# Kernel tuning notes

Hardware: AMD Instinct MI355X
Metric: run time of the kernel (lower is better)

Reference implementation:

```python
import jax, jax.numpy as jnp
import numpy as np

G, N, E, F_IN, F_OUT, C = 256, 512, 4096, 64, 64, 16


def setup_inputs() -> dict:
    key = jax.random.key(0)
    ks = jax.random.split(key, 6)
    x_batch = jax.random.normal(ks[0], (G, N, F_IN), dtype=jnp.float32)
    edge_index_batch = jax.random.randint(ks[1], (G, 2, E), 0, N, dtype=jnp.int32)
    conv_weight = jax.random.normal(ks[2], (F_OUT, F_IN), dtype=jnp.float32) * (1.0 / np.sqrt(F_IN))
    conv_bias = jax.random.normal(ks[3], (F_OUT,), dtype=jnp.float32) * 0.02
    lin_weight = jax.random.normal(ks[4], (C, F_OUT * N), dtype=jnp.float32) * (1.0 / np.sqrt(F_OUT * N))
    lin_bias = jax.random.normal(ks[5], (C,), dtype=jnp.float32) * 0.02
    return {"x_batch": x_batch, "edge_index_batch": edge_index_batch,
            "conv_weight": conv_weight, "conv_bias": conv_bias,
            "lin_weight": lin_weight, "lin_bias": lin_bias}


def _gcn_conv_graph(xw, edge_index, self_loops):
    # xw: [N, F_OUT] (already linearly transformed), edge_index: [2, E]
    row = jnp.concatenate([edge_index[0], self_loops])  # sources
    col = jnp.concatenate([edge_index[1], self_loops])  # targets
    ones = jnp.ones(row.shape[0], dtype=xw.dtype)
    deg = jax.ops.segment_sum(ones, col, num_segments=N)  # degree at target nodes
    dinv = jnp.where(deg > 0, jax.lax.rsqrt(deg), jnp.zeros_like(deg))
    norm = dinv[row] * dinv[col]                          # [E+N]
    msgs = xw[row] * norm[:, None]                        # gather + normalize
    return jax.ops.segment_sum(msgs, col, num_segments=N)  # scatter-add at targets


def reference(x_batch, edge_index_batch, conv_weight, conv_bias, lin_weight, lin_bias):
    # GCNConv (PyG defaults: self-loops, symmetric normalization, post-agg bias)
    xw = jnp.einsum('gnf,of->gno', x_batch, conv_weight)  # [G, N, F_OUT]
    self_loops = jnp.arange(N, dtype=edge_index_batch.dtype)
    h = jax.vmap(_gcn_conv_graph, in_axes=(0, 0, None))(xw, edge_index_batch, self_loops)
    h = h + conv_bias
    h = jax.nn.relu(h)
    flat = h.reshape(h.shape[0], -1)                      # [G, N*F_OUT]
    logits = flat @ lin_weight.T + lin_bias               # [G, C]
    return jax.nn.log_softmax(logits, axis=-1)
```

## Files before the change

kernel.cpp:

```cpp
#include <hip/hip_runtime.h>

#define Gn 256
#define Nn 512
#define En 4096
#define Fn 64
#define Cn 16
#define ET (En + Nn)

typedef _Float16 halfv8 __attribute__((ext_vector_type(8)));
typedef _Float16 halfv4 __attribute__((ext_vector_type(4)));
typedef _Float16 halfv2 __attribute__((ext_vector_type(2)));
typedef float    f32x4  __attribute__((ext_vector_type(4)));

__device__ __forceinline__ float pk_norm(unsigned p) {
    return (float)__builtin_bit_cast(_Float16, (unsigned short)(p & 0xffffu));
}

__global__ __launch_bounds__(256) void cvt_lw(
    const float* __restrict__ lw,
    _Float16* __restrict__ lwh)
{
    const int i = blockIdx.x * 256 + threadIdx.x;
    float4 a = *((const float4*)lw + (size_t)i * 2);
    float4 b = *((const float4*)lw + (size_t)i * 2 + 1);
    halfv8 hv;
    hv[0]=(_Float16)a.x; hv[1]=(_Float16)a.y; hv[2]=(_Float16)a.z; hv[3]=(_Float16)a.w;
    hv[4]=(_Float16)b.x; hv[5]=(_Float16)b.y; hv[6]=(_Float16)b.z; hv[7]=(_Float16)b.w;
    *(halfv8*)(lwh + (size_t)i * 8) = hv;
}

__global__ __launch_bounds__(1024, 4) void gcn_fused(
    const float* __restrict__ x,
    const int*   __restrict__ ei,
    const float* __restrict__ w,
    const float* __restrict__ wbias,
    const _Float16* __restrict__ lwh,
    const float* __restrict__ lbias,
    float* __restrict__ out)
{
    __shared__ unsigned short xs_h[Nn * Fn];
    __shared__ unsigned short xhs[Nn * Fn];
    __shared__ unsigned short wts[Fn * Fn];
    __shared__ unsigned int   epk[ET + 8];
    __shared__ float dinv[Nn];
    __shared__ int   cnt[Nn];
    __shared__ int   wsum[8];

    const int g    = blockIdx.x;
    const int tid  = threadIdx.x;
    const int lane = tid & 63;
    const int wid  = tid >> 6;

    const float* xg = x + (size_t)g * Nn * Fn;
    const int*   es = ei + (size_t)g * 2 * En;
    const int*   ed = es + En;

    const int e0s = es[tid], e1s = es[tid + 1024], e2s = es[tid + 2048], e3s = es[tid + 3072];
    const int e0t = ed[tid], e1t = ed[tid + 1024], e2t = ed[tid + 2048], e3t = ed[tid + 3072];

    if (tid < Nn) dinv[tid] = 1.0f;
    __syncthreads();

    atomicAdd(&dinv[e0t], 1.0f);
    atomicAdd(&dinv[e1t], 1.0f);
    atomicAdd(&dinv[e2t], 1.0f);
    atomicAdd(&dinv[e3t], 1.0f);

    float4 xv[8];
    #pragma unroll
    for (int it = 0; it < 8; ++it) xv[it] = *(const float4*)(xg + (tid + it * 1024) * 4);
    __syncthreads();

    int c = 0;
    if (tid < Nn) { float d = dinv[tid]; c = (int)d; dinv[tid] = rsqrtf(d); }
    int v_ = c;
    #pragma unroll
    for (int off = 1; off < 64; off <<= 1) {
        int u = __shfl_up(v_, off, 64);
        if (lane >= off) v_ += u;
    }
    if (wid < 8 && lane == 63) wsum[wid] = v_;
    __syncthreads();
    if (tid == 0) { int a = 0; for (int i = 0; i < 8; ++i) { int t = wsum[i]; wsum[i] = a; a += t; } }
    __syncthreads();
    if (tid < Nn) cnt[tid] = v_ - c + wsum[wid];
    __syncthreads();

    {
        #define FILL_EDGE(ss, tt) { \
            float nrm = dinv[ss] * dinv[tt]; \
            int slot = atomicAdd(&cnt[tt], 1); \
            unsigned short nb = __builtin_bit_cast(unsigned short, (_Float16)nrm); \
            epk[slot] = ((unsigned)(ss) << 16) | nb; }
        FILL_EDGE(e0s, e0t)
        FILL_EDGE(e1s, e1t)
        FILL_EDGE(e2s, e2t)
        FILL_EDGE(e3s, e3t)
        #undef FILL_EDGE
        if (tid < Nn) {
            float dv = dinv[tid];
            float nrm = dv * dv;
            int slot = atomicAdd(&cnt[tid], 1);
            unsigned short nb = __builtin_bit_cast(unsigned short, (_Float16)nrm);
            epk[slot] = ((unsigned)tid << 16) | nb;
        }
    }

    {
        int o = tid >> 4, f0 = (tid & 15) * 4;
        float4 v = *(const float4*)(w + o * Fn + f0);
        halfv4 hv; hv[0]=(_Float16)v.x; hv[1]=(_Float16)v.y;
                   hv[2]=(_Float16)v.z; hv[3]=(_Float16)v.w;
        int blk = f0 >> 3, hf = (f0 >> 2) & 1;
        *(halfv4*)((char*)wts + o * 128 + ((blk ^ (o & 7)) * 16) + hf * 8) = hv;
    }

    #pragma unroll
    for (int it = 0; it < 8; ++it) {
        int idx = tid + it * 1024;
        float4 v = xv[it];
        halfv4 hv; hv[0]=(_Float16)v.x; hv[1]=(_Float16)v.y;
                   hv[2]=(_Float16)v.z; hv[3]=(_Float16)v.w;
        *(halfv4*)((char*)xs_h + idx * 8) = hv;
    }
    __syncthreads();

    {
        const int qid = lane >> 4, fl = lane & 15;
        for (int r = 0; r < 8; ++r) {
            int t = r * 64 + wid * 4 + qid;
            int beg = (t == 0) ? 0 : cnt[t - 1];
            int end = cnt[t];
            float a0 = 0.f, a1 = 0.f, a2 = 0.f, a3 = 0.f;
            unsigned pA0 = epk[beg],     pA1 = epk[beg + 1];
            unsigned pA2 = epk[beg + 2], pA3 = epk[beg + 3];
            int j = beg;
            for (; j + 4 <= end; j += 4) {
                unsigned pB0 = epk[j + 4], pB1 = epk[j + 5];
                unsigned pB2 = epk[j + 6], pB3 = epk[j + 7];
                int s0 = pA0 >> 16, s1 = pA1 >> 16, s2 = pA2 >> 16, s3 = pA3 >> 16;
                float n0 = pk_norm(pA0), n1 = pk_norm(pA1);
                float n2 = pk_norm(pA2), n3 = pk_norm(pA3);
                halfv4 x0 = *(const halfv4*)((const char*)xs_h + s0 * 128 + fl * 8);
                halfv4 x1 = *(const halfv4*)((const char*)xs_h + s1 * 128 + fl * 8);
                halfv4 x2 = *(const halfv4*)((const char*)xs_h + s2 * 128 + fl * 8);
                halfv4 x3 = *(const halfv4*)((const char*)xs_h + s3 * 128 + fl * 8);
                a0 += n0 * (float)x0[0] + n1 * (float)x1[0] + n2 * (float)x2[0] + n3 * (float)x3[0];
                a1 += n0 * (float)x0[1] + n1 * (float)x1[1] + n2 * (float)x2[1] + n3 * (float)x3[1];
                a2 += n0 * (float)x0[2] + n1 * (float)x1[2] + n2 * (float)x2[2] + n3 * (float)x3[2];
                a3 += n0 * (float)x0[3] + n1 * (float)x1[3] + n2 * (float)x2[3] + n3 * (float)x3[3];
                pA0 = pB0; pA1 = pB1; pA2 = pB2; pA3 = pB3;
            }
            for (; j < end; ++j) {
                int s = pA0 >> 16;
                float nm = pk_norm(pA0);
                halfv4 xvv = *(const halfv4*)((const char*)xs_h + s * 128 + fl * 8);
                a0 += nm * (float)xvv[0]; a1 += nm * (float)xvv[1];
                a2 += nm * (float)xvv[2]; a3 += nm * (float)xvv[3];
                pA0 = pA1; pA1 = pA2; pA2 = pA3;
            }
            halfv4 hv; hv[0]=(_Float16)a0; hv[1]=(_Float16)a1;
                       hv[2]=(_Float16)a2; hv[3]=(_Float16)a3;
            int dw = t * 32 + (((fl >> 1) ^ (t & 7)) * 4) + (fl & 1) * 2;
            *(halfv4*)((char*)xhs + dw * 4) = hv;
        }
    }
    __syncthreads();

    {
        const int m = lane & 15, q = lane >> 4;
        #pragma unroll
        for (int j = 0; j < 8; ++j) {
            int idx = wid * 8 + j, tm = idx >> 2, to = idx & 3;
            int n = tm * 16 + m, o = to * 16 + m;
            halfv8 X0 = *(const halfv8*)((const char*)xhs + n * 128 + ((q       ^ (n & 7)) * 16));
            halfv8 X1 = *(const halfv8*)((const char*)xhs + n * 128 + (((4 + q) ^ (n & 7)) * 16));
            halfv8 W0 = *(const halfv8*)((const char*)wts + o * 128 + ((q       ^ (o & 7)) * 16));
            halfv8 W1 = *(const halfv8*)((const char*)wts + o * 128 + (((4 + q) ^ (o & 7)) * 16));
            f32x4 acc = {0.f, 0.f, 0.f, 0.f};
            acc = __builtin_amdgcn_mfma_f32_16x16x32_f16(W0, X0, acc, 0, 0, 0);
            acc = __builtin_amdgcn_mfma_f32_16x16x32_f16(W1, X1, acc, 0, 0, 0);
            float4 bq = *(const float4*)&wbias[to * 16 + q * 4];
            halfv4 hv;
            hv[0] = (_Float16)fmaxf(acc[0] + bq.x, 0.0f);
            hv[1] = (_Float16)fmaxf(acc[1] + bq.y, 0.0f);
            hv[2] = (_Float16)fmaxf(acc[2] + bq.z, 0.0f);
            hv[3] = (_Float16)fmaxf(acc[3] + bq.w, 0.0f);
            int sw = (to * 4 + q) ^ m;
            *(halfv4*)((char*)xs_h + n * 128 + sw * 8) = hv;
        }
    }
    __syncthreads();

    {
        const _Float16* lwc = lwh + (size_t)wid * (Nn * Fn);
        const int l7 = lane & 7, l3 = lane >> 3;
        float acc = 0.f;
        #pragma unroll 4
        for (int i = 0; i < 64; ++i) {
            int n  = i * 8 + l3;
            int rb = n << 7;
            int sA = ((l7 * 2)     ^ (n & 15));
            int sB = ((l7 * 2 + 1) ^ (n & 15));
            halfv4 hA = *(const halfv4*)((const char*)xs_h + rb + sA * 8);
            halfv4 hB = *(const halfv4*)((const char*)xs_h + rb + sB * 8);
            halfv8 wv8 = *(const halfv8*)(lwc + (n << 6) + l7 * 8);
#if __has_builtin(__builtin_amdgcn_fdot2)
            halfv2 a0; a0[0]=hA[0]; a0[1]=hA[1];
            halfv2 a1; a1[0]=hA[2]; a1[1]=hA[3];
            halfv2 a2; a2[0]=hB[0]; a2[1]=hB[1];
            halfv2 a3; a3[0]=hB[2]; a3[1]=hB[3];
            halfv2 b0; b0[0]=wv8[0]; b0[1]=wv8[1];
            halfv2 b1; b1[0]=wv8[2]; b1[1]=wv8[3];
            halfv2 b2; b2[0]=wv8[4]; b2[1]=wv8[5];
            halfv2 b3; b3[0]=wv8[6]; b3[1]=wv8[7];
            acc = __builtin_amdgcn_fdot2(a0, b0, acc, false);
            acc = __builtin_amdgcn_fdot2(a1, b1, acc, false);
            acc = __builtin_amdgcn_fdot2(a2, b2, acc, false);
            acc = __builtin_amdgcn_fdot2(a3, b3, acc, false);
#else
            acc += (float)hA[0]*(float)wv8[0] + (float)hA[1]*(float)wv8[1]
                 + (float)hA[2]*(float)wv8[2] + (float)hA[3]*(float)wv8[3]
                 + (float)hB[0]*(float)wv8[4] + (float)hB[1]*(float)wv8[5]
                 + (float)hB[2]*(float)wv8[6] + (float)hB[3]*(float)wv8[7];
#endif
        }
        #pragma unroll
        for (int off = 32; off > 0; off >>= 1) acc += __shfl_xor(acc, off, 64);
        if (lane == 0) dinv[wid] = acc;
    }
    __syncthreads();

    if (tid < Cn) {
        float v = dinv[tid] + lbias[tid];
        float m = v;
        #pragma unroll
        for (int off = 8; off > 0; off >>= 1) m = fmaxf(m, __shfl_xor(m, off, 16));
        float ex = expf(v - m);
        float ssum = ex;
        #pragma unroll
        for (int off = 8; off > 0; off >>= 1) ssum += __shfl_xor(ssum, off, 16);
        out[g * Cn + tid] = v - m - logf(ssum);
    }
}

extern "C" void kernel_launch(void* const* d_in, const int* in_sizes, int n_in,
                              void* d_out, int out_size, void* d_ws, size_t ws_size,
                              hipStream_t stream) {
    const float* x  = (const float*)d_in[0];
    const int*   ei = (const int*)d_in[1];
    const float* w  = (const float*)d_in[2];
    const float* wb = (const float*)d_in[3];
    const float* lw = (const float*)d_in[4];
    const float* lb = (const float*)d_in[5];
    float* out = (float*)d_out;

    _Float16* lwh = (_Float16*)d_ws;

    hipLaunchKernelGGL(cvt_lw, dim3(256), dim3(256), 0, stream, lw, lwh);
    hipLaunchKernelGGL(gcn_fused, dim3(Gn), dim3(1024), 0, stream,
                       x, ei, w, wb, lwh, lb, out);
}
```

Before: 112.6 us.

## Hoist global loads early, prefetch linear weights, use LDS-only barriers

Moves the x, conv weight and linear bias global loads to the start of the kernel so they overlap with the degree-count atomics. It also prefetches the first eight linear-weight vectors before the MFMA stage and keeps an eight-deep register ring buffer of them in the final dot-product loop. __syncthreads is replaced with a barrier that waits only on LDS counters, so in-flight global loads are not drained at each barrier. The final stage reads one 16-byte LDS vector per row instead of two 8-byte ones, which requires remapping weight element order. The cost is higher register pressure at 1024 threads per block, and the partial-wait barrier is correct only while no barrier-ordered dependency goes through global memory.

```diff
diff --git a/kernel.cpp b/kernel.cpp
--- a/kernel.cpp
+++ b/kernel.cpp
@@ -14,6 +14,12 @@
 
 __device__ __forceinline__ float pk_norm(unsigned p) {
     return (float)__builtin_bit_cast(_Float16, (unsigned short)(p & 0xffffu));
+}
+
+__device__ __forceinline__ void bar_lds() {
+    asm volatile("s_waitcnt lgkmcnt(0)" ::: "memory");
+    __builtin_amdgcn_s_barrier();
+    __builtin_amdgcn_sched_barrier(0);
 }
 
 __global__ __launch_bounds__(256) void cvt_lw(
@@ -57,19 +63,20 @@
 
     const int e0s = es[tid], e1s = es[tid + 1024], e2s = es[tid + 2048], e3s = es[tid + 3072];
     const int e0t = ed[tid], e1t = ed[tid + 1024], e2t = ed[tid + 2048], e3t = ed[tid + 3072];
+    float4 xv[8];
+    #pragma unroll
+    for (int it = 0; it < 8; ++it) xv[it] = *(const float4*)(xg + (tid + it * 1024) * 4);
+    const float4 wv = *(const float4*)(w + (tid >> 4) * Fn + (tid & 15) * 4);
+    const float lbv = (tid < Cn) ? lbias[tid] : 0.0f;
 
     if (tid < Nn) dinv[tid] = 1.0f;
-    __syncthreads();
+    bar_lds();
 
     atomicAdd(&dinv[e0t], 1.0f);
     atomicAdd(&dinv[e1t], 1.0f);
     atomicAdd(&dinv[e2t], 1.0f);
     atomicAdd(&dinv[e3t], 1.0f);
-
-    float4 xv[8];
-    #pragma unroll
-    for (int it = 0; it < 8; ++it) xv[it] = *(const float4*)(xg + (tid + it * 1024) * 4);
-    __syncthreads();
+    bar_lds();
 
     int c = 0;
     if (tid < Nn) { float d = dinv[tid]; c = (int)d; dinv[tid] = rsqrtf(d); }
@@ -80,11 +87,11 @@
         if (lane >= off) v_ += u;
     }
     if (wid < 8 && lane == 63) wsum[wid] = v_;
-    __syncthreads();
+    bar_lds();
     if (tid == 0) { int a = 0; for (int i = 0; i < 8; ++i) { int t = wsum[i]; wsum[i] = a; a += t; } }
-    __syncthreads();
+    bar_lds();
     if (tid < Nn) cnt[tid] = v_ - c + wsum[wid];
-    __syncthreads();
+    bar_lds();
 
     {
         #define FILL_EDGE(ss, tt) { \
@@ -108,9 +115,8 @@
 
     {
         int o = tid >> 4, f0 = (tid & 15) * 4;
-        float4 v = *(const float4*)(w + o * Fn + f0);
-        halfv4 hv; hv[0]=(_Float16)v.x; hv[1]=(_Float16)v.y;
-                   hv[2]=(_Float16)v.z; hv[3]=(_Float16)v.w;
+        halfv4 hv; hv[0]=(_Float16)wv.x; hv[1]=(_Float16)wv.y;
+                   hv[2]=(_Float16)wv.z; hv[3]=(_Float16)wv.w;
         int blk = f0 >> 3, hf = (f0 >> 2) & 1;
         *(halfv4*)((char*)wts + o * 128 + ((blk ^ (o & 7)) * 16) + hf * 8) = hv;
     }
@@ -123,7 +129,7 @@
                    hv[2]=(_Float16)v.z; hv[3]=(_Float16)v.w;
         *(halfv4*)((char*)xs_h + idx * 8) = hv;
     }
-    __syncthreads();
+    bar_lds();
 
     {
         const int qid = lane >> 4, fl = lane & 15;
@@ -165,7 +171,15 @@
             *(halfv4*)((char*)xhs + dw * 4) = hv;
         }
     }
-    __syncthreads();
+
+    const _Float16* lwc = lwh + (size_t)wid * (Nn * Fn);
+    const int l7 = lane & 7, l3 = lane >> 3;
+    const _Float16* lwp_base = lwc + l3 * 64 + l7 * 8;
+    halfv8 lwp[8];
+    #pragma unroll
+    for (int p = 0; p < 8; ++p) lwp[p] = *(const halfv8*)(lwp_base + p * 512);
+
+    bar_lds();
 
     {
         const int m = lane & 15, q = lane >> 4;
@@ -190,49 +204,46 @@
             *(halfv4*)((char*)xs_h + n * 128 + sw * 8) = hv;
         }
     }
-    __syncthreads();
-
-    {
-        const _Float16* lwc = lwh + (size_t)wid * (Nn * Fn);
-        const int l7 = lane & 7, l3 = lane >> 3;
+    bar_lds();
+
+    {
+        const int woA = (l3 & 1) * 4;
         float acc = 0.f;
-        #pragma unroll 4
+        #pragma unroll
         for (int i = 0; i < 64; ++i) {
-            int n  = i * 8 + l3;
-            int rb = n << 7;
-            int sA = ((l7 * 2)     ^ (n & 15));
-            int sB = ((l7 * 2 + 1) ^ (n & 15));
-            halfv4 hA = *(const halfv4*)((const char*)xs_h + rb + sA * 8);
-            halfv4 hB = *(const halfv4*)((const char*)xs_h + rb + sB * 8);
-            halfv8 wv8 = *(const halfv8*)(lwc + (n << 6) + l7 * 8);
+            halfv8 wv8 = lwp[i & 7];
+            if (i + 8 < 64) lwp[i & 7] = *(const halfv8*)(lwp_base + (i + 8) * 512);
+            int n   = i * 8 + l3;
+            int blk = l7 ^ ((n & 15) >> 1);
+            halfv8 H = *(const halfv8*)((const char*)xs_h + n * 128 + blk * 16);
 #if __has_builtin(__builtin_amdgcn_fdot2)
-            halfv2 a0; a0[0]=hA[0]; a0[1]=hA[1];
-            halfv2 a1; a1[0]=hA[2]; a1[1]=hA[3];
-            halfv2 a2; a2[0]=hB[0]; a2[1]=hB[1];
-            halfv2 a3; a3[0]=hB[2]; a3[1]=hB[3];
-            halfv2 b0; b0[0]=wv8[0]; b0[1]=wv8[1];
-            halfv2 b1; b1[0]=wv8[2]; b1[1]=wv8[3];
-            halfv2 b2; b2[0]=wv8[4]; b2[1]=wv8[5];
-            halfv2 b3; b3[0]=wv8[6]; b3[1]=wv8[7];
+            halfv2 a0; a0[0]=H[0]; a0[1]=H[1];
+            halfv2 a1; a1[0]=H[2]; a1[1]=H[3];
+            halfv2 a2; a2[0]=H[4]; a2[1]=H[5];
+            halfv2 a3; a3[0]=H[6]; a3[1]=H[7];
+            halfv2 b0; b0[0]=wv8[woA];         b0[1]=wv8[woA + 1];
+            halfv2 b1; b1[0]=wv8[woA + 2];     b1[1]=wv8[woA + 3];
+            halfv2 b2; b2[0]=wv8[woA ^ 4];     b2[1]=wv8[(woA ^ 4) + 1];
+            halfv2 b3; b3[0]=wv8[(woA ^ 4)+2]; b3[1]=wv8[(woA ^ 4) + 3];
             acc = __builtin_amdgcn_fdot2(a0, b0, acc, false);
             acc = __builtin_amdgcn_fdot2(a1, b1, acc, false);
             acc = __builtin_amdgcn_fdot2(a2, b2, acc, false);
             acc = __builtin_amdgcn_fdot2(a3, b3, acc, false);
 #else
-            acc += (float)hA[0]*(float)wv8[0] + (float)hA[1]*(float)wv8[1]
-                 + (float)hA[2]*(float)wv8[2] + (float)hA[3]*(float)wv8[3]
-                 + (float)hB[0]*(float)wv8[4] + (float)hB[1]*(float)wv8[5]
-                 + (float)hB[2]*(float)wv8[6] + (float)hB[3]*(float)wv8[7];
+            acc += (float)H[0]*(float)wv8[woA]       + (float)H[1]*(float)wv8[woA + 1]
+                 + (float)H[2]*(float)wv8[woA + 2]   + (float)H[3]*(float)wv8[woA + 3]
+                 + (float)H[4]*(float)wv8[woA ^ 4]   + (float)H[5]*(float)wv8[(woA ^ 4) + 1]
+                 + (float)H[6]*(float)wv8[(woA^4)+2] + (float)H[7]*(float)wv8[(woA ^ 4) + 3];
 #endif
         }
         #pragma unroll
         for (int off = 32; off > 0; off >>= 1) acc += __shfl_xor(acc, off, 64);
         if (lane == 0) dinv[wid] = acc;
     }
-    __syncthreads();
+    bar_lds();
 
     if (tid < Cn) {
-        float v = dinv[tid] + lbias[tid];
+        float v = dinv[tid] + lbv;
         float m = v;
         #pragma unroll
         for (int off = 8; off > 0; off >>= 1) m = fmaxf(m, __shfl_xor(m, off, 16));
```

Result: slower. 161.3 us (+43.2%).
